# Kernel tuning notes

Measured on AMD Instinct MI355X. Metric: run time of the kernel, lower is better.

The kernel has to match this reference:

```python
import jax, jax.numpy as jnp
from jax import lax
import numpy as np

EPS = 1e-5  # BatchNorm eps; eval-mode BN with running_mean=0, running_var=1


def _conv(x, w, b):
    return lax.conv_general_dilated(x, w, (1, 1), 'SAME', dimension_numbers=('NCHW', 'OIHW', 'NCHW')) + b[None, :, None, None]


def _cbr(x, w, b, g, a):
    # Conv -> BN(eval, mean=0, var=1) -> ReLU
    y = _conv(x, w, b)
    y = g[None, :, None, None] * (y * (1.0 / np.sqrt(1.0 + EPS))) + a[None, :, None, None]
    return jax.nn.relu(y)


def _pool(x):
    return lax.reduce_window(x, -jnp.inf, lax.max, (1, 1, 2, 2), (1, 1, 2, 2), 'VALID')


def _up2(x):
    B, C, H, W = x.shape
    Ho, Wo = 2 * H, 2 * W
    ys = jnp.arange(Ho) * ((H - 1) / (Ho - 1))
    xs = jnp.arange(Wo) * ((W - 1) / (Wo - 1))
    y0 = jnp.floor(ys).astype(jnp.int32); y1 = jnp.minimum(y0 + 1, H - 1)
    x0 = jnp.floor(xs).astype(jnp.int32); x1 = jnp.minimum(x0 + 1, W - 1)
    wy = (ys - y0).astype(x.dtype); wx = (xs - x0).astype(x.dtype)
    row = x[:, :, y0, :] * (1 - wy)[None, None, :, None] + x[:, :, y1, :] * wy[None, None, :, None]
    return row[:, :, :, x0] * (1 - wx) + row[:, :, :, x1] * wx


def _fcas(x, w, b):
    # FullyConnectedAtomicSpace: for each interior pixel (i,j) of x[0,1],
    # p = #(channel > v), n = #(channel == v), e = #(channel < v), out = (p*w0+b0 + n*w1+b1 + e*w2+b2)/3.
    # Vectorized via sort + searchsorted: O(N log N) instead of O(N^2).
    ch = x[0, 1]
    H, W = ch.shape
    flat = ch.ravel(); N = flat.size
    s = jnp.sort(flat)
    left = jnp.searchsorted(s, flat, side='left')
    right = jnp.searchsorted(s, flat, side='right')
    e = left.astype(x.dtype)            # count <
    n = (right - left).astype(x.dtype)  # count ==
    p = (N - right).astype(x.dtype)     # count >
    val = ((p * w[0] + b[0] + n * w[1] + b[1] + e * w[2] + b[2]) / 3.0).reshape(H, W)
    ii = jnp.arange(H); jj = jnp.arange(W)
    interior = ((ii >= 1) & (ii <= H - 2))[:, None] & ((jj >= 1) & (jj <= W - 2))[None, :]
    new_ch = jnp.where(interior, val, ch)
    # original converts to numpy and back -> detaches the whole tensor
    return lax.stop_gradient(x.at[0, 1].set(new_ch))


def _forward(x, w_inc, b_inc, g_inc, a_inc, w_d1, b_d1, g_d1, a_d1, w_d2, b_d2, g_d2, a_d2,
             w_d3, b_d3, g_d3, a_d3, w_u2, b_u2, g_u2, a_u2, w_u3, b_u3, g_u3, a_u3,
             w_u4, b_u4, g_u4, a_u4, w_out, b_out, fcas_w, fcas_b):
    x1 = _cbr(x, w_inc, b_inc, g_inc, a_inc)            # [B,8,512,512]
    x2 = _cbr(_pool(x1), w_d1, b_d1, g_d1, a_d1)        # [B,16,256,256]
    x3 = _cbr(_pool(x2), w_d2, b_d2, g_d2, a_d2)        # [B,32,128,128]
    x4 = _cbr(_pool(x3), w_d3, b_d3, g_d3, a_d3)        # [B,32,64,64]
    x4 = _fcas(x4, fcas_w, fcas_b)
    u = _cbr(jnp.concatenate([x3, _up2(x4)], axis=1), w_u2, b_u2, g_u2, a_u2)  # 64->16
    u = _cbr(jnp.concatenate([x2, _up2(u)], axis=1), w_u3, b_u3, g_u3, a_u3)   # 32->8
    u = _cbr(jnp.concatenate([x1, _up2(u)], axis=1), w_u4, b_u4, g_u4, a_u4)   # 16->4
    return jax.nn.sigmoid(_conv(u, w_out, b_out))       # [B,1,512,512]


def setup_inputs():
    key = jax.random.key(0)
    ks = jax.random.split(key, 24)
    d = {}
    d['x'] = jax.random.normal(ks[0], (8, 3, 512, 512), jnp.float32)
    specs = [('inc', 8, 3), ('d1', 16, 8), ('d2', 32, 16), ('d3', 32, 32), ('u2', 16, 64), ('u3', 8, 32), ('u4', 4, 16)]
    for idx, (nm, o, i) in enumerate(specs):
        k1, k2, k3, k4 = jax.random.split(ks[idx + 1], 4)
        d['w_' + nm] = jax.random.normal(k1, (o, i, 3, 3), jnp.float32) * 0.1
        d['b_' + nm] = jax.random.normal(k2, (o,), jnp.float32) * 0.1
        d['g_' + nm] = 1.0 + jax.random.normal(k3, (o,), jnp.float32) * 0.1
        d['a_' + nm] = jax.random.normal(k4, (o,), jnp.float32) * 0.1
    d['w_out'] = jax.random.normal(ks[20], (1, 4, 1, 1), jnp.float32) * 0.1
    d['b_out'] = jax.random.normal(ks[21], (1,), jnp.float32) * 0.1
    d['fcas_w'] = jnp.array([0.5, 0.5, 0.5], jnp.float32)
    d['fcas_b'] = jnp.array([0.5, 0.5, 0.5], jnp.float32)
    return d


def reference(x, w_inc, b_inc, g_inc, a_inc, w_d1, b_d1, g_d1, a_d1, w_d2, b_d2, g_d2, a_d2,
              w_d3, b_d3, g_d3, a_d3, w_u2, b_u2, g_u2, a_u2, w_u3, b_u3, g_u3, a_u3,
              w_u4, b_u4, g_u4, a_u4, w_out, b_out, fcas_w, fcas_b):
    return _forward(x, w_inc, b_inc, g_inc, a_inc, w_d1, b_d1, g_d1, a_d1, w_d2, b_d2, g_d2, a_d2,
                    w_d3, b_d3, g_d3, a_d3, w_u2, b_u2, g_u2, a_u2, w_u3, b_u3, g_u3, a_u3,
                    w_u4, b_u4, g_u4, a_u4, w_out, b_out, fcas_w, fcas_b)
```

## Files before the change

kernel.cpp:

```cpp
#include <hip/hip_runtime.h>
#include <hip/hip_bf16.h>

#define BN_RSQ 0.9999950000374997f

struct LayerP {
  const float* w; const float* b; const float* g; const float* a;
  float* wf; float* bf; int cout; int cin;
};
struct AllP { LayerP L[7]; float* zbuf; };

__global__ void prefold_kernel(AllP A) {
  LayerP p = A.L[blockIdx.y];
  int n = p.cout * p.cin * 9;
  int i = blockIdx.x * 256 + threadIdx.x;
  if (i < n) {
    int o = i / (p.cin * 9);
    p.wf[i] = p.w[i] * p.g[o] * BN_RSQ;
  }
  if (i < p.cout) p.bf[i] = p.b[i] * p.g[i] * BN_RSQ + p.a[i];
  if (blockIdx.y == 0 && blockIdx.x == 0 && i < 16) A.zbuf[i] = 0.f;
}

__device__ __forceinline__ void async_row_f32(const float* g, float* l) {
  __builtin_amdgcn_global_load_lds(
      (const __attribute__((address_space(1))) void*)g,
      (__attribute__((address_space(3))) void*)l, 4, 0, 0);
}

__global__ void up2_kernel(const float* __restrict__ in, float* __restrict__ out,
                           int Hi, int Wi) {
  const int Ho = 2 * Hi, Wo = 2 * Wi;
  const int ox = blockIdx.x * 16 + threadIdx.x;
  const int oy = blockIdx.y * 16 + threadIdx.y;
  const int bc = blockIdx.z;
  const float sy = (float)(Hi - 1) / (float)(Ho - 1);
  const float sx = (float)(Wi - 1) / (float)(Wo - 1);
  float fy = oy * sy, fx = ox * sx;
  int y0 = (int)floorf(fy); int y1 = min(y0 + 1, Hi - 1);
  int x0 = (int)floorf(fx); int x1 = min(x0 + 1, Wi - 1);
  float wy = fy - (float)y0, wx = fx - (float)x0;
  const float* p = in + (size_t)bc * Hi * Wi;
  float a00 = p[y0 * Wi + x0], a01 = p[y0 * Wi + x1];
  float a10 = p[y1 * Wi + x0], a11 = p[y1 * Wi + x1];
  float r0 = a00 * (1.f - wy) + a10 * wy;
  float r1 = a01 * (1.f - wy) + a11 * wy;
  out[((size_t)bc * Ho + oy) * Wo + ox] = r0 * (1.f - wx) + r1 * wx;
}

template <int CIN1, int CIN2, int COUTG, int OSPLIT, bool WRITE_POOL>
__launch_bounds__(256)
__global__ void conv3x3_direct(const float* __restrict__ in1,
                               const float* __restrict__ in2,
                               const float* __restrict__ wf,
                               const float* __restrict__ bf,
                               const float* __restrict__ zbuf,
                               float* __restrict__ out,
                               float* __restrict__ pout, int H, int W) {
  constexpr int CIN = CIN1 + CIN2;
  constexpr int COUT = COUTG * OSPLIT;
  __shared__ float wsm[COUTG * CIN * 12];

  const int tid = threadIdx.x;
  const int txp = (tid & 15) * 4;
  const int ty = tid >> 4;
  const int gx0 = blockIdx.x * 64;
  const int gy0 = blockIdx.y * 16;
  const int og = blockIdx.z % OSPLIT;
  const int b = blockIdx.z / OSPLIT;
  const int obase = og * COUTG;
  const int lane = tid & 63;

  for (int idx = tid; idx < COUTG * CIN * 9; idx += 256) {
    int o = idx / (CIN * 9);
    int r = idx - o * (CIN * 9);
    int c = r / 9;
    int t = r - c * 9;
    wsm[(o * CIN + c) * 12 + t] = wf[((obase + o) * CIN + c) * 9 + t];
  }
  __syncthreads();

  const int ox = gx0 + txp;
  const int oy = gy0 + ty;
  const bool vM = (oy >= 1);
  const bool vP = (oy + 1 < H);
  const float selL = (ox >= 1) ? 1.f : 0.f;
  const float selR = (ox + 4 < W) ? 1.f : 0.f;
  const float* zp = zbuf + 4 - (size_t)ox;

  float acc[COUTG][4];
#pragma unroll
  for (int o = 0; o < COUTG; ++o)
#pragma unroll
    for (int i = 0; i < 4; ++i) acc[o][i] = 0.f;

  auto body = [&](const float* __restrict__ plane, int cabs) {
    const float* rC = plane + (size_t)oy * W;
    const float* rM = vM ? (rC - W) : zp;
    const float* rP = vP ? (rC + W) : zp;
    float rr[3][6];
#pragma unroll
    for (int dy = 0; dy < 3; ++dy) {
      const float* p = (dy == 0 ? rM : (dy == 1 ? rC : rP)) + ox;
      float4 v4 = *(const float4*)p;
      float lm = p[-1];
      float rp = p[4];
      rr[dy][0] = lm * selL;
      rr[dy][1] = v4.x; rr[dy][2] = v4.y; rr[dy][3] = v4.z; rr[dy][4] = v4.w;
      rr[dy][5] = rp * selR;
    }
#pragma unroll
    for (int o = 0; o < COUTG; ++o) {
      const float4* wp = (const float4*)&wsm[(o * CIN + cabs) * 12];
      float4 wa = wp[0];
      float4 wb = wp[1];
      float w8 = wsm[(o * CIN + cabs) * 12 + 8];
#pragma unroll
      for (int i = 0; i < 4; ++i) {
        float s = acc[o][i];
        s = fmaf(rr[0][i + 0], wa.x, s);
        s = fmaf(rr[0][i + 1], wa.y, s);
        s = fmaf(rr[0][i + 2], wa.z, s);
        s = fmaf(rr[1][i + 0], wa.w, s);
        s = fmaf(rr[1][i + 1], wb.x, s);
        s = fmaf(rr[1][i + 2], wb.y, s);
        s = fmaf(rr[2][i + 0], wb.z, s);
        s = fmaf(rr[2][i + 1], wb.w, s);
        s = fmaf(rr[2][i + 2], w8, s);
        acc[o][i] = s;
      }
    }
  };

#pragma unroll 1
  for (int c = 0; c < CIN1; ++c)
    body(in1 + (size_t)(b * CIN1 + c) * H * W, c);
  if (CIN2 > 0) {
#pragma unroll 1
    for (int c = 0; c < CIN2; ++c)
      body(in2 + (size_t)(b * CIN2 + c) * H * W, CIN1 + c);
  }

  const int H2 = H >> 1, W2 = W >> 1;
#pragma unroll
  for (int o = 0; o < COUTG; ++o) {
    float bo = bf[obase + o];
    float rv[4];
#pragma unroll
    for (int i = 0; i < 4; ++i) rv[i] = fmaxf(acc[o][i] + bo, 0.f);
    *(float4*)&out[((size_t)(b * COUT + obase + o) * H + oy) * W + ox] =
        *(float4*)rv;
    if (WRITE_POOL) {
      float m0 = fmaxf(rv[0], rv[1]);
      float m1 = fmaxf(rv[2], rv[3]);
      float q0 = fmaxf(m0, __shfl_down(m0, 16));
      float q1 = fmaxf(m1, __shfl_down(m1, 16));
      if (((lane >> 4) & 1) == 0) {
        float2 pw; pw.x = q0; pw.y = q1;
        *(float2*)&pout[((size_t)(b * COUT + obase + o) * H2 + (oy >> 1)) * W2 +
                        (ox >> 1)] = pw;
      }
    }
  }
}

__launch_bounds__(256)
__global__ void conv3x3_u4(const float* __restrict__ in1,
                           const float* __restrict__ in2,
                           const float* __restrict__ wf,
                           const float* __restrict__ bf,
                           const float* __restrict__ wout,
                           const float* __restrict__ bout,
                           const float* __restrict__ zbuf,
                           float* __restrict__ out) {
  constexpr int H = 512, W = 512, Hi = 256, Wi = 256;
  constexpr int CIN1 = 8, CIN2 = 8, CIN = 16, COUT = 4;
  __shared__ float utile[CIN2][18][68];
  __shared__ float4 w4i2[COUT * CIN2][2];
  __shared__ float w8i2[COUT * CIN2];

  const int tid = threadIdx.x;
  const int lane = tid & 63;
  const int wv = tid >> 6;
  const int txp = (tid & 15) * 4;
  const int ty = tid >> 4;
  const int gx0 = blockIdx.x * 64;
  const int gy0 = blockIdx.y * 16;
  const int b = blockIdx.z;

  if (tid < COUT * CIN2) {
    const int o = tid >> 3, cc = tid & 7;
    const float* wp = wf + (o * CIN + CIN1 + cc) * 9;
    w4i2[tid][0] = make_float4(wp[0], wp[1], wp[2], wp[3]);
    w4i2[tid][1] = make_float4(wp[4], wp[5], wp[6], wp[7]);
    w8i2[tid] = wp[8];
  }

  const float sx = (float)(Wi - 1) / (float)(W - 1);
  const float sy = (float)(Hi - 1) / (float)(H - 1);
  const float* in2b = in2 + (size_t)b * CIN2 * Hi * Wi;

  {
    const int gox = gx0 + lane;
    const float fx = gox * sx;
    const int x0 = (int)fx;
    const int x1i = min(x0 + 1, Wi - 1);
    const float wx = fx - (float)x0;
    for (int t5 = wv; t5 < CIN2 * 18; t5 += 4) {
      const int c = t5 / 18;
      const int yy = t5 - c * 18;
      const int goy = gy0 + yy - 1;
      float v = 0.f;
      if (goy >= 0 && goy < H) {
        const float fy = goy * sy;
        const int y0 = (int)fy;
        const int y1 = min(y0 + 1, Hi - 1);
        const float wy = fy - (float)y0;
        const float* p0 = in2b + ((size_t)c * Hi + y0) * Wi;
        const float* p1 = in2b + ((size_t)c * Hi + y1) * Wi;
        float a00 = p0[x0], a01 = p0[x1i];
        float a10 = p1[x0], a11 = p1[x1i];
        float r0 = a00 * (1.f - wy) + a10 * wy;
        float r1 = a01 * (1.f - wy) + a11 * wy;
        v = r0 * (1.f - wx) + r1 * wx;
      }
      utile[c][yy][1 + lane] = v;
    }
  }
  for (int i = tid; i < 2 * CIN2 * 18; i += 256) {
    const int side = i & 1;
    const int row = i >> 1;
    const int c = row / 18;
    const int yy = row - c * 18;
    const int gox = side ? (gx0 + 64) : (gx0 - 1);
    const int goy = gy0 + yy - 1;
    float v = 0.f;
    if (goy >= 0 && goy < H && gox >= 0 && gox < W) {
      const float fy = goy * sy;
      const float fx = gox * sx;
      const int y0 = (int)fy;
      const int y1 = min(y0 + 1, Hi - 1);
      const int x0 = (int)fx;
      const int x1i = min(x0 + 1, Wi - 1);
      const float wy = fy - (float)y0;
      const float wx = fx - (float)x0;
      const float* p = in2b + (size_t)c * Hi * Wi;
      float a00 = p[y0 * Wi + x0], a01 = p[y0 * Wi + x1i];
      float a10 = p[y1 * Wi + x0], a11 = p[y1 * Wi + x1i];
      float r0 = a00 * (1.f - wy) + a10 * wy;
      float r1 = a01 * (1.f - wy) + a11 * wy;
      v = r0 * (1.f - wx) + r1 * wx;
    }
    utile[c][yy][side ? 65 : 0] = v;
  }
  __syncthreads();

  const int ox = gx0 + txp;
  const int oy = gy0 + ty;
  const bool vM = (oy >= 1);
  const bool vP = (oy + 1 < H);
  const float selL = (ox >= 1) ? 1.f : 0.f;
  const float selR = (ox + 4 < W) ? 1.f : 0.f;
  const float* zp = zbuf + 4 - (size_t)ox;

  float acc[COUT][4];
#pragma unroll
  for (int o = 0; o < COUT; ++o)
#pragma unroll
    for (int i = 0; i < 4; ++i) acc[o][i] = 0.f;

#pragma unroll 1
  for (int c = 0; c < CIN1; ++c) {
    const float* plane = in1 + (size_t)(b * CIN1 + c) * H * W;
    const float* rC = plane + (size_t)oy * W;
    const float* rM = vM ? (rC - W) : zp;
    const float* rP = vP ? (rC + W) : zp;
    float rr[3][6];
#pragma unroll
    for (int dy = 0; dy < 3; ++dy) {
      const float* p = (dy == 0 ? rM : (dy == 1 ? rC : rP)) + ox;
      float4 v4 = *(const float4*)p;
      float lm = p[-1];
      float rp = p[4];
      rr[dy][0] = lm * selL;
      rr[dy][1] = v4.x; rr[dy][2] = v4.y; rr[dy][3] = v4.z; rr[dy][4] = v4.w;
      rr[dy][5] = rp * selR;
    }
#pragma unroll
    for (int o = 0; o < COUT; ++o) {
      const float* wp = wf + (o * CIN + c) * 9;
      float w0 = wp[0], w1 = wp[1], w2 = wp[2], w3 = wp[3], w4 = wp[4];
      float w5 = wp[5], w6 = wp[6], w7 = wp[7], w8 = wp[8];
#pragma unroll
      for (int i = 0; i < 4; ++i) {
        float s = acc[o][i];
        s = fmaf(rr[0][i + 0], w0, s);
        s = fmaf(rr[0][i + 1], w1, s);
        s = fmaf(rr[0][i + 2], w2, s);
        s = fmaf(rr[1][i + 0], w3, s);
        s = fmaf(rr[1][i + 1], w4, s);
        s = fmaf(rr[1][i + 2], w5, s);
        s = fmaf(rr[2][i + 0], w6, s);
        s = fmaf(rr[2][i + 1], w7, s);
        s = fmaf(rr[2][i + 2], w8, s);
        acc[o][i] = s;
      }
    }
  }

#pragma unroll
  for (int c = 0; c < CIN2; ++c) {
    float rr[3][6];
#pragma unroll
    for (int dy = 0; dy < 3; ++dy) {
      const float* p = &utile[c][ty + dy][txp];
      float4 a4 = *(const float4*)p;
      float2 b2 = *(const float2*)(p + 4);
      rr[dy][0] = a4.x; rr[dy][1] = a4.y; rr[dy][2] = a4.z; rr[dy][3] = a4.w;
      rr[dy][4] = b2.x; rr[dy][5] = b2.y;
    }
#pragma unroll
    for (int o = 0; o < COUT; ++o) {
      const int pr = o * CIN2 + c;
      float4 wa = w4i2[pr][0];
      float4 wb = w4i2[pr][1];
      float w8 = w8i2[pr];
#pragma unroll
      for (int i = 0; i < 4; ++i) {
        float s = acc[o][i];
        s = fmaf(rr[0][i + 0], wa.x, s);
        s = fmaf(rr[0][i + 1], wa.y, s);
        s = fmaf(rr[0][i + 2], wa.z, s);
        s = fmaf(rr[1][i + 0], wa.w, s);
        s = fmaf(rr[1][i + 1], wb.x, s);
        s = fmaf(rr[1][i + 2], wb.y, s);
        s = fmaf(rr[2][i + 0], wb.z, s);
        s = fmaf(rr[2][i + 1], wb.w, s);
        s = fmaf(rr[2][i + 2], w8, s);
        acc[o][i] = s;
      }
    }
  }

  float sv[4];
#pragma unroll
  for (int i = 0; i < 4; ++i) sv[i] = bout[0];
#pragma unroll
  for (int o = 0; o < COUT; ++o) {
    float bo = bf[o], wo = wout[o];
#pragma unroll
    for (int i = 0; i < 4; ++i) {
      float rr2 = fmaxf(acc[o][i] + bo, 0.f);
      sv[i] = fmaf(rr2, wo, sv[i]);
    }
  }
#pragma unroll
  for (int i = 0; i < 4; ++i) sv[i] = 1.f / (1.f + __expf(-sv[i]));
  *(float4*)&out[((size_t)b * H + oy) * W + ox] = *(float4*)sv;
}

template <int CIN1, int CIN2, int COUTG, int OSPLIT, bool UP_IN2, bool FUSE_OUT,
          bool WRITE_POOL>
__launch_bounds__(256)
__global__ void conv3x3_cbr(const float* __restrict__ in1,
                            const float* __restrict__ in2,
                            const float* __restrict__ wf,
                            const float* __restrict__ bf,
                            const float* __restrict__ wout,
                            const float* __restrict__ bout,
                            float* __restrict__ out,
                            float* __restrict__ pout, int H, int W) {
  constexpr int CIN = CIN1 + CIN2;
  constexpr int COUT = COUTG * OSPLIT;
  constexpr int PPT = 4;
  constexpr int CHUNK = (CIN < 4) ? CIN : 4;
  constexpr int XS = 68;
  constexpr int YT = 18;
  constexpr int ROWS = CHUNK * YT;

  __shared__ float tile[CHUNK][YT][XS];
  __shared__ float wsm[COUTG * CIN * 12];

  const int tid = threadIdx.x;
  const int txp = (tid & 15) * PPT;
  const int ty = tid >> 4;
  const int gx0 = blockIdx.x * 64;
  const int gy0 = blockIdx.y * 16;
  const int b = blockIdx.z & 7;
  const int og = blockIdx.z >> 3;
  const int obase = og * COUTG;

  const int lane = tid & 63;
  const int wv = tid >> 6;

  const int Hi = H >> 1, Wi = W >> 1;
  const float syf = UP_IN2 ? (float)(Hi - 1) / (float)(H - 1) : 0.f;

  int ux0 = 0, ux1 = 0;
  float uwx = 0.f;
  if (UP_IN2) {
    const float sx = (float)(Wi - 1) / (float)(W - 1);
    float fx = (gx0 + lane) * sx;
    ux0 = (int)fx;
    ux1 = min(ux0 + 1, Wi - 1);
    uwx = fx - (float)ux0;
  }

  for (int idx = tid; idx < COUTG * CIN * 9; idx += 256) {
    int o = idx / (CIN * 9);
    int r = idx - o * (CIN * 9);
    int c = r / 9;
    int t = r - c * 9;
    wsm[(o * CIN + c) * 12 + t] = wf[((obase + o) * CIN + c) * 9 + t];
  }

  float acc[COUTG][PPT];
#pragma unroll
  for (int o = 0; o < COUTG; ++o)
#pragma unroll
    for (int i = 0; i < PPT; ++i) acc[o][i] = 0.f;

  for (int cc = 0; cc < CIN; cc += CHUNK) {
    __syncthreads();
    if (wv < CHUNK) {
      const int c = wv;
      const int cg = cc + c;
      const bool dir1 = (CIN2 == 0 || cg < CIN1);
      if (dir1 || !UP_IN2) {
        const float* src;
        int cb;
        if (dir1) { src = in1; cb = b * CIN1 + cg; }
        else      { src = in2; cb = b * CIN2 + (cg - CIN1); }
        const float* base =
            src + (size_t)cb * H * W + (size_t)(gy0 - 1) * W + gx0 + lane;
#pragma unroll
        for (int yy = 0; yy < YT; ++yy) {
          const int iy = gy0 + yy - 1;
          if (iy >= 0 && iy < H) {
            async_row_f32(base + (size_t)yy * W, &tile[c][yy][1]);
          } else {
            tile[c][yy][1 + lane] = 0.f;
          }
        }
      } else {
        const int cb = b * CIN2 + (cg - CIN1);
#pragma unroll 1
        for (int yy = 0; yy < YT; ++yy) {
          const int iy = gy0 + yy - 1;
          float v = 0.f;
          if (iy >= 0 && iy < H) {
            float fy = iy * syf;
            int y0 = (int)fy;
            int y1 = min(y0 + 1, Hi - 1);
            float wy = fy - (float)y0;
            const float* r0p = in2 + (size_t)(cb * Hi + y0) * Wi;
            const float* r1p = in2 + (size_t)(cb * Hi + y1) * Wi;
            float a00 = r0p[ux0], a01 = r0p[ux1];
            float a10 = r1p[ux0], a11 = r1p[ux1];
            float r0 = a00 * (1.f - wy) + a10 * wy;
            float r1 = a01 * (1.f - wy) + a11 * wy;
            v = r0 * (1.f - uwx) + r1 * uwx;
          }
          tile[c][yy][1 + lane] = v;
        }
      }
    }
    for (int idx = tid; idx < 2 * ROWS; idx += 256) {
      const int row = idx >> 1;
      const int side = idx & 1;
      const int c = row / YT;
      const int yy = row - c * YT;
      const int iy = gy0 + yy - 1;
      const int ix = side ? (gx0 + 64) : (gx0 - 1);
      const int cg = cc + c;
      float v = 0.f;
      if (iy >= 0 && iy < H && ix >= 0 && ix < W) {
        if (CIN2 == 0 || cg < CIN1) {
          const int cb = b * CIN1 + cg;
          v = in1[(size_t)(cb * H + iy) * W + ix];
        } else if (UP_IN2) {
          const int cb = b * CIN2 + (cg - CIN1);
          const float sx = (float)(Wi - 1) / (float)(W - 1);
          float fy = iy * syf, fx = ix * sx;
          int y0 = (int)fy; int y1 = min(y0 + 1, Hi - 1);
          int x0 = (int)fx; int x1 = min(x0 + 1, Wi - 1);
          float wy = fy - (float)y0, wx = fx - (float)x0;
          const float* p = in2 + (size_t)cb * Hi * Wi;
          float a00 = p[y0 * Wi + x0], a01 = p[y0 * Wi + x1];
          float a10 = p[y1 * Wi + x0], a11 = p[y1 * Wi + x1];
          float r0 = a00 * (1.f - wy) + a10 * wy;
          float r1 = a01 * (1.f - wy) + a11 * wy;
          v = r0 * (1.f - wx) + r1 * wx;
        } else {
          const int cb = b * CIN2 + (cg - CIN1);
          v = in2[(size_t)(cb * H + iy) * W + ix];
        }
      }
      tile[c][yy][side ? 65 : 0] = v;
    }
    __syncthreads();
#pragma unroll
    for (int c = 0; c < CHUNK; ++c) {
      float rr[3][6];
#pragma unroll
      for (int dy = 0; dy < 3; ++dy) {
        const float* p = &tile[c][ty + dy][txp];
        float4 a4 = *(const float4*)p;
        float2 b2 = *(const float2*)(p + 4);
        rr[dy][0] = a4.x; rr[dy][1] = a4.y; rr[dy][2] = a4.z; rr[dy][3] = a4.w;
        rr[dy][4] = b2.x; rr[dy][5] = b2.y;
      }
      const int cabs = cc + c;
#pragma unroll
      for (int o = 0; o < COUTG; ++o) {
        const float4* wp = (const float4*)&wsm[(o * CIN + cabs) * 12];
        float4 wa = wp[0];
        float4 wb = wp[1];
        float w8 = wsm[(o * CIN + cabs) * 12 + 8];
#pragma unroll
        for (int i = 0; i < PPT; ++i) {
          float s = acc[o][i];
          s = fmaf(rr[0][i + 0], wa.x, s);
          s = fmaf(rr[0][i + 1], wa.y, s);
          s = fmaf(rr[0][i + 2], wa.z, s);
          s = fmaf(rr[1][i + 0], wa.w, s);
          s = fmaf(rr[1][i + 1], wb.x, s);
          s = fmaf(rr[1][i + 2], wb.y, s);
          s = fmaf(rr[2][i + 0], wb.z, s);
          s = fmaf(rr[2][i + 1], wb.w, s);
          s = fmaf(rr[2][i + 2], w8, s);
          acc[o][i] = s;
        }
      }
    }
  }

  const int oy = gy0 + ty;
  const int ox = gx0 + txp;
  if (FUSE_OUT) {
    float sv[PPT];
#pragma unroll
    for (int i = 0; i < PPT; ++i) sv[i] = bout[0];
#pragma unroll
    for (int o = 0; o < COUTG; ++o) {
      float bo = bf[obase + o], wo = wout[o];
#pragma unroll
      for (int i = 0; i < PPT; ++i) {
        float rr2 = fmaxf(acc[o][i] + bo, 0.f);
        sv[i] = fmaf(rr2, wo, sv[i]);
      }
    }
#pragma unroll
    for (int i = 0; i < PPT; ++i) sv[i] = 1.f / (1.f + __expf(-sv[i]));
    *(float4*)&out[((size_t)b * H + oy) * W + ox] = *(float4*)sv;
  } else {
    const int H2 = H >> 1, W2 = W >> 1;
#pragma unroll
    for (int o = 0; o < COUTG; ++o) {
      float bo = bf[obase + o];
      float rv[PPT];
#pragma unroll
      for (int i = 0; i < PPT; ++i) rv[i] = fmaxf(acc[o][i] + bo, 0.f);
      *(float4*)&out[((size_t)(b * COUT + obase + o) * H + oy) * W + ox] =
          *(float4*)rv;
      if (WRITE_POOL) {
        float m0 = fmaxf(rv[0], rv[1]);
        float m1 = fmaxf(rv[2], rv[3]);
        float q0 = fmaxf(m0, __shfl_down(m0, 16));
        float q1 = fmaxf(m1, __shfl_down(m1, 16));
        if (((lane >> 4) & 1) == 0) {
          float2 pw; pw.x = q0; pw.y = q1;
          *(float2*)&pout[((size_t)(b * COUT + obase + o) * H2 + (oy >> 1)) * W2 +
                          (ox >> 1)] = pw;
        }
      }
    }
  }
}

__global__ void fcas_partial(const float* __restrict__ ch,
                             int* __restrict__ pcnt, int* __restrict__ ncnt) {
  __shared__ float sv[256];
  const int e = blockIdx.x * 256 + threadIdx.x;
  const int s = blockIdx.y;
  sv[threadIdx.x] = ch[s * 256 + threadIdx.x];
  __syncthreads();
  const float v = ch[e];
  int p = 0, n = 0;
#pragma unroll 4
  for (int k = 0; k < 256; ++k) {
    float u = sv[k];
    p += (u > v);
    n += (u == v);
  }
  pcnt[s * 4096 + e] = p;
  ncnt[s * 4096 + e] = n;
}

__global__ void fcas_final(float* __restrict__ ch,
                           const int* __restrict__ pcnt,
                           const int* __restrict__ ncnt,
                           const float* __restrict__ w,
                           const float* __restrict__ bb) {
  const int e = blockIdx.x * 256 + threadIdx.x;
  int p = 0, n = 0;
#pragma unroll
  for (int s = 0; s < 16; ++s) {
    p += pcnt[s * 4096 + e];
    n += ncnt[s * 4096 + e];
  }
  const int el = 4096 - p - n;
  float val = ((float)p * w[0] + bb[0] + (float)n * w[1] + bb[1] +
               (float)el * w[2] + bb[2]) / 3.0f;
  int i = e >> 6, j = e & 63;
  bool interior = (i >= 1) && (i <= 62) && (j >= 1) && (j <= 62);
  if (interior) ch[e] = val;
}

extern "C" void kernel_launch(void* const* d_in, const int* in_sizes, int n_in,
                              void* d_out, int out_size, void* d_ws, size_t ws_size,
                              hipStream_t stream) {
  const float* x      = (const float*)d_in[0];
  const float* w_inc  = (const float*)d_in[1];
  const float* b_inc  = (const float*)d_in[2];
  const float* g_inc  = (const float*)d_in[3];
  const float* a_inc  = (const float*)d_in[4];
  const float* w_d1   = (const float*)d_in[5];
  const float* b_d1   = (const float*)d_in[6];
  const float* g_d1   = (const float*)d_in[7];
  const float* a_d1   = (const float*)d_in[8];
  const float* w_d2   = (const float*)d_in[9];
  const float* b_d2   = (const float*)d_in[10];
  const float* g_d2   = (const float*)d_in[11];
  const float* a_d2   = (const float*)d_in[12];
  const float* w_d3   = (const float*)d_in[13];
  const float* b_d3   = (const float*)d_in[14];
  const float* g_d3   = (const float*)d_in[15];
  const float* a_d3   = (const float*)d_in[16];
  const float* w_u2   = (const float*)d_in[17];
  const float* b_u2   = (const float*)d_in[18];
  const float* g_u2   = (const float*)d_in[19];
  const float* a_u2   = (const float*)d_in[20];
  const float* w_u3   = (const float*)d_in[21];
  const float* b_u3   = (const float*)d_in[22];
  const float* g_u3   = (const float*)d_in[23];
  const float* a_u3   = (const float*)d_in[24];
  const float* w_u4   = (const float*)d_in[25];
  const float* b_u4   = (const float*)d_in[26];
  const float* g_u4   = (const float*)d_in[27];
  const float* a_u4   = (const float*)d_in[28];
  const float* w_out  = (const float*)d_in[29];
  const float* b_out  = (const float*)d_in[30];
  const float* fcas_w = (const float*)d_in[31];
  const float* fcas_b = (const float*)d_in[32];

  float* ws = (float*)d_ws;
  float* zbuf   = ws;
  float* wf_inc = ws + 16;
  float* wf_d1  = wf_inc + 216;
  float* wf_d2  = wf_d1 + 1152;
  float* wf_d3  = wf_d2 + 4608;
  float* wf_u2  = wf_d3 + 9216;
  float* wf_u3  = wf_u2 + 9216;
  float* wf_u4  = wf_u3 + 2304;
  float* bf_inc = wf_u4 + 576;
  float* bf_d1  = bf_inc + 8;
  float* bf_d2  = bf_d1 + 16;
  float* bf_d3  = bf_d2 + 32;
  float* bf_u2  = bf_d3 + 32;
  float* bf_u3  = bf_u2 + 16;
  float* bf_u4  = bf_u3 + 8;
  int*   pcnt   = (int*)(ws + 27424);
  int*   ncnt   = pcnt + 65536;
  float* x1  = (float*)(ncnt + 65536);
  float* p1  = x1 + 16777216;
  float* x2  = p1 + 4194304;
  float* p2  = x2 + 8388608;
  float* x3  = p2 + 2097152;
  float* p3  = x3 + 4194304;
  float* x4  = p3 + 1048576;
  float* upa = x4 + 1048576;
  float* uo2 = upa + 4194304;
  float* uo3 = uo2 + 2097152;
  float* upb = x3;
  float* outp = (float*)d_out;

  AllP A;
  A.L[0] = {w_inc, b_inc, g_inc, a_inc, wf_inc, bf_inc, 8, 3};
  A.L[1] = {w_d1, b_d1, g_d1, a_d1, wf_d1, bf_d1, 16, 8};
  A.L[2] = {w_d2, b_d2, g_d2, a_d2, wf_d2, bf_d2, 32, 16};
  A.L[3] = {w_d3, b_d3, g_d3, a_d3, wf_d3, bf_d3, 32, 32};
  A.L[4] = {w_u2, b_u2, g_u2, a_u2, wf_u2, bf_u2, 16, 64};
  A.L[5] = {w_u3, b_u3, g_u3, a_u3, wf_u3, bf_u3, 8, 32};
  A.L[6] = {w_u4, b_u4, g_u4, a_u4, wf_u4, bf_u4, 4, 16};
  A.zbuf = zbuf;
  prefold_kernel<<<dim3(36, 7), dim3(256), 0, stream>>>(A);

  dim3 blk(256);
  dim3 blk2(16, 16);

  conv3x3_cbr<3, 0, 8, 1, false, false, true><<<dim3(8, 32, 8), blk, 0, stream>>>(
      x, nullptr, wf_inc, bf_inc, nullptr, nullptr, x1, p1, 512, 512);
  conv3x3_direct<8, 0, 4, 4, true><<<dim3(4, 16, 32), blk, 0, stream>>>(
      p1, nullptr, wf_d1, bf_d1, zbuf, x2, p2, 256, 256);
  conv3x3_direct<16, 0, 4, 8, true><<<dim3(2, 8, 64), blk, 0, stream>>>(
      p2, nullptr, wf_d2, bf_d2, zbuf, x3, p3, 128, 128);
  conv3x3_direct<32, 0, 2, 16, false><<<dim3(1, 4, 128), blk, 0, stream>>>(
      p3, nullptr, wf_d3, bf_d3, zbuf, x4, nullptr, 64, 64);
  fcas_partial<<<dim3(16, 16), blk, 0, stream>>>(x4 + 4096, pcnt, ncnt);
  fcas_final<<<dim3(16), blk, 0, stream>>>(x4 + 4096, pcnt, ncnt, fcas_w, fcas_b);
  up2_kernel<<<dim3(8, 8, 256), blk2, 0, stream>>>(x4, upa, 64, 64);
  conv3x3_direct<32, 32, 4, 4, false><<<dim3(2, 8, 32), blk, 0, stream>>>(
      x3, upa, wf_u2, bf_u2, zbuf, uo2, nullptr, 128, 128);
  up2_kernel<<<dim3(16, 16, 128), blk2, 0, stream>>>(uo2, upb, 128, 128);
  conv3x3_direct<16, 16, 4, 2, false><<<dim3(4, 16, 16), blk, 0, stream>>>(
      x2, upb, wf_u3, bf_u3, zbuf, uo3, nullptr, 256, 256);
  conv3x3_u4<<<dim3(8, 32, 8), blk, 0, stream>>>(
      x1, uo3, wf_u4, bf_u4, w_out, b_out, zbuf, outp);
}
```

Baseline: 434.3 us.

## Split upsampled-skip tile into two channel phases to halve LDS in u4 conv

After: 444.5 us. +2.3%, slower.

```diff
diff --git a/kernel.cpp b/kernel.cpp
--- a/kernel.cpp
+++ b/kernel.cpp
@@ -174,7 +174,8 @@
                            float* __restrict__ out) {
   constexpr int H = 512, W = 512, Hi = 256, Wi = 256;
   constexpr int CIN1 = 8, CIN2 = 8, CIN = 16, COUT = 4;
-  __shared__ float utile[CIN2][18][68];
+  constexpr int CH = 4;
+  __shared__ float utile[CH][18][68];
   __shared__ float4 w4i2[COUT * CIN2][2];
   __shared__ float w8i2[COUT * CIN2];
 
@@ -199,13 +200,48 @@
   const float sy = (float)(Hi - 1) / (float)(H - 1);
   const float* in2b = in2 + (size_t)b * CIN2 * Hi * Wi;
 
-  {
-    const int gox = gx0 + lane;
-    const float fx = gox * sx;
-    const int x0 = (int)fx;
-    const int x1i = min(x0 + 1, Wi - 1);
-    const float wx = fx - (float)x0;
-    for (int t5 = wv; t5 < CIN2 * 18; t5 += 4) {
+  const float fxL = (float)(gx0 + lane) * sx;
+  const int x0L = (int)fxL;
+  const int x1L = min(x0L + 1, Wi - 1);
+  const float wxL = fxL - (float)x0L;
+
+  const int hside = tid & 1;
+  const int hrow = tid >> 1;
+  const int hc = hrow / 18;
+  const int hyy = hrow - hc * 18;
+  const int hgox = hside ? (gx0 + 64) : (gx0 - 1);
+  const int hgoy = gy0 + hyy - 1;
+  const bool hin = (hgoy >= 0) && (hgoy < H) && (hgox >= 0) && (hgox < W);
+  const int hgoyc = min(max(hgoy, 0), H - 1);
+  const float hfy = (float)hgoyc * sy;
+  const int hy0 = (int)hfy;
+  const int hy1 = min(hy0 + 1, Hi - 1);
+  const float hwy = hfy - (float)hy0;
+  const float hfx = (float)min(max(hgox, 0), W - 1) * sx;
+  const int hx0 = (int)hfx;
+  const int hx1 = min(hx0 + 1, Wi - 1);
+  const float hwx = hfx - (float)hx0;
+
+  const int ox = gx0 + txp;
+  const int oy = gy0 + ty;
+  const bool vM = (oy >= 1);
+  const bool vP = (oy + 1 < H);
+  const float selL = (ox >= 1) ? 1.f : 0.f;
+  const float selR = (ox + 4 < W) ? 1.f : 0.f;
+  const float* zp = zbuf + 4 - (size_t)ox;
+
+  float acc[COUT][4];
+#pragma unroll
+  for (int o = 0; o < COUT; ++o)
+#pragma unroll
+    for (int i = 0; i < 4; ++i) acc[o][i] = 0.f;
+
+#pragma unroll 1
+  for (int ph = 0; ph < 2; ++ph) {
+    const int cbase = ph * CH;
+    if (ph) __syncthreads();
+
+    for (int t5 = wv; t5 < CH * 18; t5 += 4) {
       const int c = t5 / 18;
       const int yy = t5 - c * 18;
       const int goy = gy0 + yy - 1;
@@ -215,128 +251,103 @@
         const int y0 = (int)fy;
         const int y1 = min(y0 + 1, Hi - 1);
         const float wy = fy - (float)y0;
-        const float* p0 = in2b + ((size_t)c * Hi + y0) * Wi;
-        const float* p1 = in2b + ((size_t)c * Hi + y1) * Wi;
-        float a00 = p0[x0], a01 = p0[x1i];
-        float a10 = p1[x0], a11 = p1[x1i];
+        const float* p0 = in2b + ((size_t)(cbase + c) * Hi + y0) * Wi;
+        const float* p1 = in2b + ((size_t)(cbase + c) * Hi + y1) * Wi;
+        float a00 = p0[x0L], a01 = p0[x1L];
+        float a10 = p1[x0L], a11 = p1[x1L];
         float r0 = a00 * (1.f - wy) + a10 * wy;
         float r1 = a01 * (1.f - wy) + a11 * wy;
-        v = r0 * (1.f - wx) + r1 * wx;
+        v = r0 * (1.f - wxL) + r1 * wxL;
       }
       utile[c][yy][1 + lane] = v;
     }
-  }
-  for (int i = tid; i < 2 * CIN2 * 18; i += 256) {
-    const int side = i & 1;
-    const int row = i >> 1;
-    const int c = row / 18;
-    const int yy = row - c * 18;
-    const int gox = side ? (gx0 + 64) : (gx0 - 1);
-    const int goy = gy0 + yy - 1;
-    float v = 0.f;
-    if (goy >= 0 && goy < H && gox >= 0 && gox < W) {
-      const float fy = goy * sy;
-      const float fx = gox * sx;
-      const int y0 = (int)fy;
-      const int y1 = min(y0 + 1, Hi - 1);
-      const int x0 = (int)fx;
-      const int x1i = min(x0 + 1, Wi - 1);
-      const float wy = fy - (float)y0;
-      const float wx = fx - (float)x0;
-      const float* p = in2b + (size_t)c * Hi * Wi;
-      float a00 = p[y0 * Wi + x0], a01 = p[y0 * Wi + x1i];
-      float a10 = p[y1 * Wi + x0], a11 = p[y1 * Wi + x1i];
-      float r0 = a00 * (1.f - wy) + a10 * wy;
-      float r1 = a01 * (1.f - wy) + a11 * wy;
-      v = r0 * (1.f - wx) + r1 * wx;
-    }
-    utile[c][yy][side ? 65 : 0] = v;
-  }
-  __syncthreads();
-
-  const int ox = gx0 + txp;
-  const int oy = gy0 + ty;
-  const bool vM = (oy >= 1);
-  const bool vP = (oy + 1 < H);
-  const float selL = (ox >= 1) ? 1.f : 0.f;
-  const float selR = (ox + 4 < W) ? 1.f : 0.f;
-  const float* zp = zbuf + 4 - (size_t)ox;
-
-  float acc[COUT][4];
-#pragma unroll
-  for (int o = 0; o < COUT; ++o)
-#pragma unroll
-    for (int i = 0; i < 4; ++i) acc[o][i] = 0.f;
-
+    if (tid < 2 * CH * 18) {
+      float v = 0.f;
+      if (hin) {
+        const float* pc = in2b + (size_t)(cbase + hc) * (Hi * Wi);
+        float a00 = pc[hy0 * Wi + hx0], a01 = pc[hy0 * Wi + hx1];
+        float a10 = pc[hy1 * Wi + hx0], a11 = pc[hy1 * Wi + hx1];
+        float r0 = a00 * (1.f - hwy) + a10 * hwy;
+        float r1 = a01 * (1.f - hwy) + a11 * hwy;
+        v = r0 * (1.f - hwx) + r1 * hwx;
+      }
+      utile[hc][hyy][hside ? 65 : 0] = v;
+    }
+    __syncthreads();
+
+    if (ph == 0) {
 #pragma unroll 1
-  for (int c = 0; c < CIN1; ++c) {
-    const float* plane = in1 + (size_t)(b * CIN1 + c) * H * W;
-    const float* rC = plane + (size_t)oy * W;
-    const float* rM = vM ? (rC - W) : zp;
-    const float* rP = vP ? (rC + W) : zp;
-    float rr[3][6];
-#pragma unroll
-    for (int dy = 0; dy < 3; ++dy) {
-      const float* p = (dy == 0 ? rM : (dy == 1 ? rC : rP)) + ox;
-      float4 v4 = *(const float4*)p;
-      float lm = p[-1];
-      float rp = p[4];
-      rr[dy][0] = lm * selL;
-      rr[dy][1] = v4.x; rr[dy][2] = v4.y; rr[dy][3] = v4.z; rr[dy][4] = v4.w;
-      rr[dy][5] = rp * selR;
-    }
-#pragma unroll
-    for (int o = 0; o < COUT; ++o) {
-      const float* wp = wf + (o * CIN + c) * 9;
-      float w0 = wp[0], w1 = wp[1], w2 = wp[2], w3 = wp[3], w4 = wp[4];
-      float w5 = wp[5], w6 = wp[6], w7 = wp[7], w8 = wp[8];
-#pragma unroll
-      for (int i = 0; i < 4; ++i) {
-        float s = acc[o][i];
-        s = fmaf(rr[0][i + 0], w0, s);
-        s = fmaf(rr[0][i + 1], w1, s);
-        s = fmaf(rr[0][i + 2], w2, s);
-        s = fmaf(rr[1][i + 0], w3, s);
-        s = fmaf(rr[1][i + 1], w4, s);
-        s = fmaf(rr[1][i + 2], w5, s);
-        s = fmaf(rr[2][i + 0], w6, s);
-        s = fmaf(rr[2][i + 1], w7, s);
-        s = fmaf(rr[2][i + 2], w8, s);
-        acc[o][i] = s;
-      }
-    }
-  }
-
-#pragma unroll
-  for (int c = 0; c < CIN2; ++c) {
-    float rr[3][6];
-#pragma unroll
-    for (int dy = 0; dy < 3; ++dy) {
-      const float* p = &utile[c][ty + dy][txp];
-      float4 a4 = *(const float4*)p;
-      float2 b2 = *(const float2*)(p + 4);
-      rr[dy][0] = a4.x; rr[dy][1] = a4.y; rr[dy][2] = a4.z; rr[dy][3] = a4.w;
-      rr[dy][4] = b2.x; rr[dy][5] = b2.y;
-    }
-#pragma unroll
-    for (int o = 0; o < COUT; ++o) {
-      const int pr = o * CIN2 + c;
-      float4 wa = w4i2[pr][0];
-      float4 wb = w4i2[pr][1];
-      float w8 = w8i2[pr];
-#pragma unroll
-      for (int i = 0; i < 4; ++i) {
-        float s = acc[o][i];
-        s = fmaf(rr[0][i + 0], wa.x, s);
-        s = fmaf(rr[0][i + 1], wa.y, s);
-        s = fmaf(rr[0][i + 2], wa.z, s);
-        s = fmaf(rr[1][i + 0], wa.w, s);
-        s = fmaf(rr[1][i + 1], wb.x, s);
-        s = fmaf(rr[1][i + 2], wb.y, s);
-        s = fmaf(rr[2][i + 0], wb.z, s);
-        s = fmaf(rr[2][i + 1], wb.w, s);
-        s = fmaf(rr[2][i + 2], w8, s);
-        acc[o][i] = s;
+      for (int c = 0; c < CIN1; ++c) {
+        const float* plane = in1 + (size_t)(b * CIN1 + c) * H * W;
+        const float* rC = plane + (size_t)oy * W;
+        const float* rM = vM ? (rC - W) : zp;
+        const float* rP = vP ? (rC + W) : zp;
+        float rr[3][6];
+#pragma unroll
+        for (int dy = 0; dy < 3; ++dy) {
+          const float* p = (dy == 0 ? rM : (dy == 1 ? rC : rP)) + ox;
+          float4 v4 = *(const float4*)p;
+          float lm = p[-1];
+          float rp = p[4];
+          rr[dy][0] = lm * selL;
+          rr[dy][1] = v4.x; rr[dy][2] = v4.y; rr[dy][3] = v4.z; rr[dy][4] = v4.w;
+          rr[dy][5] = rp * selR;
+        }
+#pragma unroll
+        for (int o = 0; o < COUT; ++o) {
+          const float* wp = wf + (o * CIN + c) * 9;
+          float w0 = wp[0], w1 = wp[1], w2 = wp[2], w3 = wp[3], w4 = wp[4];
+          float w5 = wp[5], w6 = wp[6], w7 = wp[7], w8 = wp[8];
+#pragma unroll
+          for (int i = 0; i < 4; ++i) {
+            float s = acc[o][i];
+            s = fmaf(rr[0][i + 0], w0, s);
+            s = fmaf(rr[0][i + 1], w1, s);
+            s = fmaf(rr[0][i + 2], w2, s);
+            s = fmaf(rr[1][i + 0], w3, s);
+            s = fmaf(rr[1][i + 1], w4, s);
+            s = fmaf(rr[1][i + 2], w5, s);
+            s = fmaf(rr[2][i + 0], w6, s);
+            s = fmaf(rr[2][i + 1], w7, s);
+            s = fmaf(rr[2][i + 2], w8, s);
+            acc[o][i] = s;
+          }
+        }
+      }
+    }
+
+#pragma unroll
+    for (int c = 0; c < CH; ++c) {
+      float rr[3][6];
+#pragma unroll
+      for (int dy = 0; dy < 3; ++dy) {
+        const float* p = &utile[c][ty + dy][txp];
+        float4 a4 = *(const float4*)p;
+        float2 b2 = *(const float2*)(p + 4);
+        rr[dy][0] = a4.x; rr[dy][1] = a4.y; rr[dy][2] = a4.z; rr[dy][3] = a4.w;
+        rr[dy][4] = b2.x; rr[dy][5] = b2.y;
+      }
+      const int cr = cbase + c;
+#pragma unroll
+      for (int o = 0; o < COUT; ++o) {
+        const int pr = o * CIN2 + cr;
+        float4 wa = w4i2[pr][0];
+        float4 wb = w4i2[pr][1];
+        float w8 = w8i2[pr];
+#pragma unroll
+        for (int i = 0; i < 4; ++i) {
+          float s = acc[o][i];
+          s = fmaf(rr[0][i + 0], wa.x, s);
+          s = fmaf(rr[0][i + 1], wa.y, s);
+          s = fmaf(rr[0][i + 2], wa.z, s);
+          s = fmaf(rr[1][i + 0], wa.w, s);
+          s = fmaf(rr[1][i + 1], wb.x, s);
+          s = fmaf(rr[1][i + 2], wb.y, s);
+          s = fmaf(rr[2][i + 0], wb.z, s);
+          s = fmaf(rr[2][i + 1], wb.w, s);
+          s = fmaf(rr[2][i + 2], w8, s);
+          acc[o][i] = s;
+        }
       }
     }
   }
```
